# Kernel tuning notes

Measured on AMD Instinct MI355X. Metric: run time of the kernel, lower is better.

Reference implementation:

```python
import jax, jax.numpy as jnp
import numpy as np

H = 16
D_MODEL = 1024
D_HID = 50  # hidden width of the 1->50->1 mask MLP


def setup_inputs() -> dict:
    key = jax.random.key(0)
    ks = jax.random.split(key, 16)
    B, S, D = 16, 768, D_MODEL
    n, nk = 512, 256  # code length n, redundancy n-k; S = n + nk
    inp = {
        "query": jax.random.normal(ks[0], (B, S, D), jnp.float32),
        "key": jax.random.normal(ks[1], (B, S, D), jnp.float32),
        "value": jax.random.normal(ks[2], (B, S, D), jnp.float32),
        "pc_matrix": jax.random.uniform(ks[3], (nk, n), jnp.float32),
        # four Linear(d_model, d_model) layers: q, k, v, out. Stored so that y = x @ W + b.
        "Wq": jax.random.normal(ks[4], (D, D), jnp.float32) * 0.02,
        "bq": jnp.zeros((D,), jnp.float32),
        "Wk": jax.random.normal(ks[5], (D, D), jnp.float32) * 0.02,
        "bk": jnp.zeros((D,), jnp.float32),
        "Wv": jax.random.normal(ks[6], (D, D), jnp.float32) * 0.02,
        "bv": jnp.zeros((D,), jnp.float32),
        "Wo": jax.random.normal(ks[7], (D, D), jnp.float32) * 0.02,
        "bo": jnp.zeros((D,), jnp.float32),
        # one_d_mapping: Linear(1,50) -> ReLU -> Linear(50,1)
        "mw1": jax.random.normal(ks[8], (1, D_HID), jnp.float32) * 0.5,
        "mb1": jax.random.normal(ks[9], (D_HID,), jnp.float32) * 0.1,
        "mw2": jax.random.normal(ks[10], (D_HID, 1), jnp.float32) * 0.5,
        "mb2": jnp.zeros((1,), jnp.float32),
    }
    return inp


def _mask_from_pc(pc, mw1, mb1, mw2, mb2):
    # pc: (nk, n). Build (S, S) block matrix, S = n + nk.
    nknk = pc @ pc.T            # (nk, nk)
    nn = pc.T @ pc              # (n, n)
    top = jnp.concatenate([nn, pc.T], axis=1)     # (n, S)
    bot = jnp.concatenate([pc, nknk], axis=1)     # (nk, S)
    M = jnp.concatenate([top, bot], axis=0)       # (S, S)
    # elementwise 1->50->1 MLP
    h = jax.nn.relu(M[..., None] * mw1[0] + mb1)  # (S, S, 50)
    out = h @ mw2 + mb2                           # (S, S, 1)
    return out[..., 0]                            # (S, S)


def reference(query, key, value, pc_matrix, Wq, bq, Wk, bk, Wv, bv, Wo, bo,
              mw1, mb1, mw2, mb2):
    B, S, D = query.shape
    dk = D // H
    q = (query @ Wq + bq).reshape(B, S, H, dk).transpose(0, 2, 1, 3)
    k = (key @ Wk + bk).reshape(B, S, H, dk).transpose(0, 2, 1, 3)
    v = (value @ Wv + bv).reshape(B, S, H, dk).transpose(0, 2, 1, 3)
    scores = jnp.einsum("bhqd,bhkd->bhqk", q, k) / jnp.sqrt(jnp.float32(dk))
    mask = _mask_from_pc(pc_matrix, mw1, mb1, mw2, mb2)  # (S, S)
    scores = scores * mask[None, None]  # multiplicative float mask
    p = jax.nn.softmax(scores, axis=-1)  # dropout is identity in eval mode
    x = jnp.einsum("bhqk,bhkd->bhqd", p, v)
    x = x.transpose(0, 2, 1, 3).reshape(B, S, D)
    return x @ Wo + bo
```

## Files before the change

### kernel.cpp

```cpp
#include <hip/hip_runtime.h>
#include <stdint.h>

typedef _Float16 f16;
typedef _Float16 f16x8 __attribute__((ext_vector_type(8)));
typedef float f32x4 __attribute__((ext_vector_type(4)));

union U4 { uint4 u; f16 h[8]; };
union U2 { uint2 u; f16 h[4]; };

#define GLOAD16(g, l)                                                         \
  __builtin_amdgcn_global_load_lds(                                           \
      (const __attribute__((address_space(1))) void*)(g),                     \
      (__attribute__((address_space(3))) void*)(l), 16, 0, 0)

__global__ __launch_bounds__(256) void k_wt(const float* __restrict__ W0,
                                            const float* __restrict__ W1,
                                            const float* __restrict__ W2,
                                            const float* __restrict__ W3,
                                            f16* __restrict__ T0, f16* __restrict__ T1,
                                            f16* __restrict__ T2, f16* __restrict__ T3) {
    __shared__ f16 tile[64 * 65];
    int z = blockIdx.z;
    const float* W = z == 0 ? W0 : z == 1 ? W1 : z == 2 ? W2 : W3;
    f16* Wt = z == 0 ? T0 : z == 1 ? T1 : z == 2 ? T2 : T3;
    int t = threadIdx.x;
    int k0 = blockIdx.x * 64, n0 = blockIdx.y * 64;
    #pragma unroll
    for (int i = 0; i < 4; i++) {
        int cid = t + i * 256;
        int row = cid >> 4, c4 = cid & 15;
        float4 v = *(const float4*)(W + (size_t)(k0 + row) * 1024 + n0 + c4 * 4);
        tile[(c4 * 4 + 0) * 65 + row] = (f16)v.x;
        tile[(c4 * 4 + 1) * 65 + row] = (f16)v.y;
        tile[(c4 * 4 + 2) * 65 + row] = (f16)v.z;
        tile[(c4 * 4 + 3) * 65 + row] = (f16)v.w;
    }
    __syncthreads();
    #pragma unroll
    for (int i = 0; i < 2; i++) {
        int cid = t + i * 256;
        int nr = cid >> 3, kc = cid & 7;
        U4 u;
        #pragma unroll
        for (int j = 0; j < 8; j++) u.h[j] = tile[nr * 65 + kc * 8 + j];
        *(uint4*)(Wt + (size_t)(n0 + nr) * 1024 + k0 + kc * 8) = u.u;
    }
}

__global__ __launch_bounds__(256) void k_cvt(const float* __restrict__ in,
                                             f16* __restrict__ out) {
    size_t id = (size_t)blockIdx.x * 256 + threadIdx.x;
    float4 a = *(const float4*)(in + id * 8);
    float4 b = *(const float4*)(in + id * 8 + 4);
    U4 u;
    u.h[0] = (f16)a.x; u.h[1] = (f16)a.y; u.h[2] = (f16)a.z; u.h[3] = (f16)a.w;
    u.h[4] = (f16)b.x; u.h[5] = (f16)b.y; u.h[6] = (f16)b.z; u.h[7] = (f16)b.w;
    *(uint4*)(out + id * 8) = u.u;
}

template <int TRANS>
__global__ __launch_bounds__(256) void k_gram(const float* __restrict__ pc,
                                              float* __restrict__ out) {
    constexpr int N = TRANS ? 256 : 512;
    constexpr int K = TRANS ? 512 : 256;
    __shared__ float As[16][68];
    __shared__ float Bs[16][68];
    int t = threadIdx.x;
    int i0 = blockIdx.x * 64, j0 = blockIdx.y * 64;
    int ty = t >> 4, tx = t & 15;
    float acc[4][4];
    #pragma unroll
    for (int r = 0; r < 4; r++)
        #pragma unroll
        for (int c = 0; c < 4; c++) acc[r][c] = 0.f;

    for (int kt = 0; kt < K; kt += 16) {
        if (TRANS == 0) {
            int k = t >> 4, c4 = t & 15;
            float4 va = *(const float4*)(pc + (size_t)(kt + k) * 512 + i0 + c4 * 4);
            float4 vb = *(const float4*)(pc + (size_t)(kt + k) * 512 + j0 + c4 * 4);
            *(float4*)&As[k][c4 * 4] = va;
            *(float4*)&Bs[k][c4 * 4] = vb;
        } else {
            int r = t >> 2, kc = t & 3;
            float4 va = *(const float4*)(pc + (size_t)(i0 + r) * 512 + kt + kc * 4);
            As[kc * 4 + 0][r] = va.x; As[kc * 4 + 1][r] = va.y;
            As[kc * 4 + 2][r] = va.z; As[kc * 4 + 3][r] = va.w;
            float4 vb = *(const float4*)(pc + (size_t)(j0 + r) * 512 + kt + kc * 4);
            Bs[kc * 4 + 0][r] = vb.x; Bs[kc * 4 + 1][r] = vb.y;
            Bs[kc * 4 + 2][r] = vb.z; Bs[kc * 4 + 3][r] = vb.w;
        }
        __syncthreads();
        #pragma unroll
        for (int u = 0; u < 16; u++) {
            float4 av = *(const float4*)&As[u][ty * 4];
            float4 bv = *(const float4*)&Bs[u][tx * 4];
            float aa[4] = {av.x, av.y, av.z, av.w};
            float bb[4] = {bv.x, bv.y, bv.z, bv.w};
            #pragma unroll
            for (int r = 0; r < 4; r++)
                #pragma unroll
                for (int c = 0; c < 4; c++) acc[r][c] += aa[r] * bb[c];
        }
        __syncthreads();
    }
    #pragma unroll
    for (int r = 0; r < 4; r++)
        #pragma unroll
        for (int c = 0; c < 4; c++)
            out[(size_t)(i0 + ty * 4 + r) * N + j0 + tx * 4 + c] = acc[r][c];
}

__global__ __launch_bounds__(256) void k_mask(const float* __restrict__ pc,
                                              const float* __restrict__ nn,
                                              const float* __restrict__ nknk,
                                              const float* __restrict__ mw1,
                                              const float* __restrict__ mb1,
                                              const float* __restrict__ mw2,
                                              const float* __restrict__ mb2,
                                              float* __restrict__ maskp) {
    __shared__ float w1[50], b1[50], w2[50];
    int t = threadIdx.x;
    if (t < 50) { w1[t] = mw1[t]; b1[t] = mb1[t]; w2[t] = mw2[t]; }
    __syncthreads();
    int id = blockIdx.x * 256 + t;
    int i = id / 768, j = id - i * 768;
    float M;
    if (i < 512) M = (j < 512) ? nn[(size_t)i * 512 + j] : pc[(size_t)(j - 512) * 512 + i];
    else         M = (j < 512) ? pc[(size_t)(i - 512) * 512 + j]
                               : nknk[(size_t)(i - 512) * 256 + (j - 512)];
    float acc = mb2[0];
    #pragma unroll 10
    for (int u = 0; u < 50; u++) acc += fmaxf(M * w1[u] + b1[u], 0.f) * w2[u];
    maskp[id] = acc * 0.18033688011112042f;
}

__global__ __launch_bounds__(256) void k_vt(const f16* __restrict__ Vh,
                                            f16* __restrict__ VT) {
    __shared__ f16 tile[64][72];
    int t = threadIdx.x;
    int s0 = blockIdx.x * 64;
    int bh = blockIdx.y, b = bh >> 4, h = bh & 15;
    #pragma unroll
    for (int p = 0; p < 2; p++) {
        int cid = t + p * 256;
        int s = cid >> 3, dc = cid & 7;
        *(uint4*)&tile[s][dc * 8] =
            *(const uint4*)(Vh + ((size_t)b * 768 + s0 + s) * 1024 + h * 64 + dc * 8);
    }
    __syncthreads();
    #pragma unroll
    for (int p = 0; p < 2; p++) {
        int cid = t + p * 256;
        int d = cid >> 3, sc = cid & 7;
        U4 u;
        #pragma unroll
        for (int j = 0; j < 8; j++) u.h[j] = tile[sc * 8 + j][d];
        *(uint4*)(VT + ((size_t)bh * 64 + d) * 768 + s0 + sc * 8) = u.u;
    }
}

template <int MODE>
__global__ __launch_bounds__(256) void k_gemm(const f16* __restrict__ A,
                                              const f16* __restrict__ Bt,
                                              const float* __restrict__ bias,
                                              void* out0v, void* out1v) {
    __shared__ f16 As[128 * 32];
    __shared__ f16 Bs[128 * 32];
    int t = threadIdx.x;
    int w = t >> 6, lane = t & 63, l15 = lane & 15, quad = lane >> 4;
    int wm = w >> 1, wn = w & 1;
    int id = blockIdx.x;
    int rest = id >> 3;
    int row0 = ((id & 7) * 12 + rest % 12) * 128;
    int n0 = (rest / 12) * 128;

    int m0 = w * 16 + (lane >> 2);
    int m1 = m0 + 64;
    int ks0 = (lane & 3) ^ ((m0 >> 1) & 3);
    int ks1 = (lane & 3) ^ ((m1 >> 1) & 3);
    const f16* gA0 = A + (size_t)(row0 + m0) * 1024 + ks0 * 8;
    const f16* gA1 = A + (size_t)(row0 + m1) * 1024 + ks1 * 8;
    const f16* gB0 = Bt + (size_t)(n0 + m0) * 1024 + ks0 * 8;
    const f16* gB1 = Bt + (size_t)(n0 + m1) * 1024 + ks1 * 8;
    f16* lA = As + w * 512;
    f16* lB = Bs + w * 512;
    int sw = (l15 >> 1) & 3;

    f32x4 acc[4][4];
    #pragma unroll
    for (int mi = 0; mi < 4; mi++)
        #pragma unroll
        for (int ni = 0; ni < 4; ni++) acc[mi][ni] = (f32x4){0.f, 0.f, 0.f, 0.f};

    for (int kt = 0; kt < 32; kt++) {
        int k0 = kt * 32;
        GLOAD16(gA0 + k0, lA);
        GLOAD16(gA1 + k0, lA + 2048);
        GLOAD16(gB0 + k0, lB);
        GLOAD16(gB1 + k0, lB + 2048);
        __syncthreads();
        f16x8 af[4], bf_[4];
        #pragma unroll
        for (int mi = 0; mi < 4; mi++)
            af[mi] = *(const f16x8*)((const char*)As +
                     (size_t)(wm * 64 + mi * 16 + l15) * 64 + ((quad ^ sw) << 4));
        #pragma unroll
        for (int ni = 0; ni < 4; ni++)
            bf_[ni] = *(const f16x8*)((const char*)Bs +
                      (size_t)(wn * 64 + ni * 16 + l15) * 64 + ((quad ^ sw) << 4));
        #pragma unroll
        for (int mi = 0; mi < 4; mi++)
            #pragma unroll
            for (int ni = 0; ni < 4; ni++)
                acc[mi][ni] = __builtin_amdgcn_mfma_f32_16x16x32_f16(af[mi], bf_[ni],
                                                                     acc[mi][ni], 0, 0, 0);
        __syncthreads();
    }
    #pragma unroll
    for (int mi = 0; mi < 4; mi++) {
        #pragma unroll
        for (int ni = 0; ni < 4; ni++) {
            int col = n0 + wn * 64 + ni * 16 + l15;
            float bv = bias[col];
            #pragma unroll
            for (int r = 0; r < 4; r++) {
                int row = row0 + wm * 64 + mi * 16 + quad * 4 + r;
                float v = acc[mi][ni][r] + bv;
                size_t idx = (size_t)row * 1024 + col;
                if (MODE == 0) {
                    ((f16*)out0v)[idx] = (f16)v;
                } else if (MODE == 1) {
                    f16 hi = (f16)v;
                    ((f16*)out0v)[idx] = hi;
                    ((f16*)out1v)[idx] = (f16)(v - (float)hi);
                } else {
                    ((float*)out0v)[idx] = v;
                }
            }
        }
    }
}

__global__ __launch_bounds__(256) void k_attn(const f16* __restrict__ Qhi,
                                              const f16* __restrict__ Qlo,
                                              const f16* __restrict__ Khi,
                                              const f16* __restrict__ Klo,
                                              const f16* __restrict__ VT,
                                              const float* __restrict__ maskp,
                                              f16* __restrict__ Xout) {
    __shared__ f16 Ksh[2][64 * 64];
    __shared__ f16 Ksl[2][64 * 64];
    __shared__ f16 Vs[2][64 * 64];
    __shared__ f16 Ps[4][16 * 64];
    int t = threadIdx.x;
    int w = t >> 6, lane = t & 63, l15 = lane & 15, quad = lane >> 4;
    int id = blockIdx.x;
    int bh = (id & 7) + ((id >> 3) / 12) * 8;
    int q0 = ((id >> 3) % 12) * 64;
    int b = bh >> 4, h = bh & 15;
    const size_t base = ((size_t)b * 768) * 1024 + h * 64;

    int srow = lane >> 3;
    int sslot = lane & 7;

    f16x8 qh[2], ql[2];
    int qrow = q0 + w * 16 + l15;
    #pragma unroll
    for (int c = 0; c < 2; c++) {
        qh[c] = *(const f16x8*)(Qhi + base + (size_t)qrow * 1024 + c * 32 + quad * 8);
        ql[c] = *(const f16x8*)(Qlo + base + (size_t)qrow * 1024 + c * 32 + quad * 8);
    }
    float mrow = -1e30f, lrow = 0.f;
    f32x4 o[4];
    #pragma unroll
    for (int ni = 0; ni < 4; ni++) o[ni] = (f32x4){0.f, 0.f, 0.f, 0.f};

    auto STAGE = [&](int bsel, int k0) {
        #pragma unroll
        for (int p = 0; p < 2; p++) {
            int row = w * 16 + p * 8 + srow;
            int ss = sslot ^ (row & 7);
            GLOAD16(Khi + base + (size_t)(k0 + row) * 1024 + ss * 8,
                    &Ksh[bsel][w * 1024 + p * 512]);
            GLOAD16(Klo + base + (size_t)(k0 + row) * 1024 + ss * 8,
                    &Ksl[bsel][w * 1024 + p * 512]);
            GLOAD16(VT + ((size_t)bh * 64 + row) * 768 + k0 + ss * 8,
                    &Vs[bsel][w * 1024 + p * 512]);
        }
    };

    STAGE(0, 0);
    __syncthreads();
    int buf = 0;
    int kx = l15 & 7;
    const float* mbase = maskp + (size_t)quad * 4 * 768 + q0 + w * 16 + l15;

    for (int kt = 0; kt < 12; kt++) {
        int k0 = kt * 64;
        float mvs[4][4];
        #pragma unroll
        for (int kn = 0; kn < 4; kn++)
            #pragma unroll
            for (int r = 0; r < 4; r++)
                mvs[kn][r] = mbase[(size_t)(k0 + kn * 16 + r) * 768];
        if (kt < 11) STAGE(buf ^ 1, k0 + 64);

        float sv[4][4];
        #pragma unroll
        for (int kn = 0; kn < 4; kn++) {
            f32x4 s = (f32x4){0.f, 0.f, 0.f, 0.f};
            int key = kn * 16 + l15;
            #pragma unroll
            for (int c = 0; c < 2; c++) {
                int slot = ((c << 2) + quad) ^ kx;
                f16x8 kh = *(const f16x8*)((const char*)&Ksh[buf][0] +
                                           (size_t)key * 128 + (slot << 4));
                f16x8 kl = *(const f16x8*)((const char*)&Ksl[buf][0] +
                                           (size_t)key * 128 + (slot << 4));
                s = __builtin_amdgcn_mfma_f32_16x16x32_f16(kh, qh[c], s, 0, 0, 0);
                s = __builtin_amdgcn_mfma_f32_16x16x32_f16(kh, ql[c], s, 0, 0, 0);
                s = __builtin_amdgcn_mfma_f32_16x16x32_f16(kl, qh[c], s, 0, 0, 0);
            }
            #pragma unroll
            for (int r = 0; r < 4; r++) sv[kn][r] = s[r] * mvs[kn][r];
        }

        float tk0 = fmaxf(fmaxf(sv[0][0], sv[0][1]), fmaxf(sv[0][2], sv[0][3]));
        float tk1 = fmaxf(fmaxf(sv[1][0], sv[1][1]), fmaxf(sv[1][2], sv[1][3]));
        float tk2 = fmaxf(fmaxf(sv[2][0], sv[2][1]), fmaxf(sv[2][2], sv[2][3]));
        float tk3 = fmaxf(fmaxf(sv[3][0], sv[3][1]), fmaxf(sv[3][2], sv[3][3]));
        float tm = fmaxf(fmaxf(tk0, tk1), fmaxf(tk2, tk3));
        tm = fmaxf(tm, __shfl_xor(tm, 16));
        tm = fmaxf(tm, __shfl_xor(tm, 32));
        if (__any(tm > mrow + 11.0f)) {
            float mn = fmaxf(mrow, tm);
            float alpha = exp2f(mrow - mn);
            mrow = mn;
            lrow *= alpha;
            #pragma unroll
            for (int ni = 0; ni < 4; ni++)
                #pragma unroll
                for (int r = 0; r < 4; r++) o[ni][r] *= alpha;
        }
        float rs = 0.f;
        #pragma unroll
        for (int kn = 0; kn < 4; kn++) {
            U2 pk;
            #pragma unroll
            for (int r = 0; r < 4; r++) {
                float pv = exp2f(sv[kn][r] - mrow);
                rs += pv;
                pk.h[r] = (f16)pv;
            }
            int slot = (kn * 2 + (quad >> 1)) ^ kx;
            *(uint2*)((char*)&Ps[w][0] + l15 * 128 + (slot << 4) + ((quad & 1) << 3)) = pk.u;
        }
        rs += __shfl_xor(rs, 16);
        rs += __shfl_xor(rs, 32);
        lrow += rs;

        asm volatile("s_waitcnt lgkmcnt(0)" ::: "memory");
        __builtin_amdgcn_sched_barrier(0);
        #pragma unroll
        for (int c = 0; c < 2; c++) {
            int pslot = ((c << 2) + quad) ^ kx;
            f16x8 pa = *(const f16x8*)((const char*)&Ps[w][0] +
                                       (size_t)l15 * 128 + (pslot << 4));
            #pragma unroll
            for (int ni = 0; ni < 4; ni++) {
                int d = ni * 16 + l15;
                f16x8 vb = *(const f16x8*)((const char*)&Vs[buf][0] +
                                           (size_t)d * 128 + (pslot << 4));
                o[ni] = __builtin_amdgcn_mfma_f32_16x16x32_f16(vb, pa, o[ni], 0, 0, 0);
            }
        }
        __syncthreads();
        buf ^= 1;
    }
    float rl = 1.0f / lrow;
    int qg = q0 + w * 16 + l15;
    #pragma unroll
    for (int ni = 0; ni < 4; ni++) {
        U2 ok;
        #pragma unroll
        for (int r = 0; r < 4; r++) ok.h[r] = (f16)(o[ni][r] * rl);
        *(uint2*)(Xout + ((size_t)b * 768 + qg) * 1024 + h * 64 + ni * 16 + quad * 4) = ok.u;
    }
}

extern "C" void kernel_launch(void* const* d_in, const int* in_sizes, int n_in,
                              void* d_out, int out_size, void* d_ws, size_t ws_size,
                              hipStream_t stream) {
    (void)in_sizes; (void)n_in; (void)out_size; (void)ws_size;
    const float* query = (const float*)d_in[0];
    const float* key   = (const float*)d_in[1];
    const float* value = (const float*)d_in[2];
    const float* pc    = (const float*)d_in[3];
    const float* Wq    = (const float*)d_in[4];
    const float* bq    = (const float*)d_in[5];
    const float* Wk    = (const float*)d_in[6];
    const float* bk    = (const float*)d_in[7];
    const float* Wv    = (const float*)d_in[8];
    const float* bv    = (const float*)d_in[9];
    const float* Wo    = (const float*)d_in[10];
    const float* bo    = (const float*)d_in[11];
    const float* mw1   = (const float*)d_in[12];
    const float* mb1   = (const float*)d_in[13];
    const float* mw2   = (const float*)d_in[14];
    const float* mb2   = (const float*)d_in[15];

    char* p = (char*)d_ws;
    auto take = [&](size_t bytes) -> char* {
        char* r = p; p += (bytes + 255) & ~(size_t)255; return r;
    };
    const size_t NTOK = 12288, DM = 1024;
    float* maskb = (float*)take(768 * 768 * 4);
    float* nnb   = (float*)take(512 * 512 * 4);
    float* nknkb = (float*)take(256 * 256 * 4);
    f16* Wqt = (f16*)take(DM * DM * 2);
    f16* Wkt = (f16*)take(DM * DM * 2);
    f16* Wvt = (f16*)take(DM * DM * 2);
    f16* Wot = (f16*)take(DM * DM * 2);
    f16* buf1 = (f16*)take(NTOK * DM * 2);
    f16* Qhi = (f16*)take(NTOK * DM * 2);
    f16* Qlo = (f16*)take(NTOK * DM * 2);
    f16* Khi = (f16*)take(NTOK * DM * 2);
    f16* Klo = (f16*)take(NTOK * DM * 2);
    f16* Vhb = (f16*)take(NTOK * DM * 2);
    f16* VTb = (f16*)take(NTOK * DM * 2);

    k_wt<<<dim3(16, 16, 4), 256, 0, stream>>>(Wq, Wk, Wv, Wo, Wqt, Wkt, Wvt, Wot);
    k_gram<0><<<dim3(8, 8), 256, 0, stream>>>(pc, nnb);
    k_gram<1><<<dim3(4, 4), 256, 0, stream>>>(pc, nknkb);
    k_mask<<<2304, 256, 0, stream>>>(pc, nnb, nknkb, mw1, mb1, mw2, mb2, maskb);

    k_cvt<<<6144, 256, 0, stream>>>(query, buf1);
    k_gemm<1><<<768, 256, 0, stream>>>(buf1, Wqt, bq, Qhi, Qlo);
    k_cvt<<<6144, 256, 0, stream>>>(key, buf1);
    k_gemm<1><<<768, 256, 0, stream>>>(buf1, Wkt, bk, Khi, Klo);
    k_cvt<<<6144, 256, 0, stream>>>(value, buf1);
    k_gemm<0><<<768, 256, 0, stream>>>(buf1, Wvt, bv, Vhb, nullptr);

    k_vt<<<dim3(12, 256), 256, 0, stream>>>(Vhb, VTb);

    k_attn<<<3072, 256, 0, stream>>>(Qhi, Qlo, Khi, Klo, VTb, maskb, buf1);

    k_gemm<2><<<768, 256, 0, stream>>>(buf1, Wot, bo, d_out, nullptr);
}
```

Measured before the change: 606.6 us.

## Single-buffer V tile and load it within the iteration to cut LDS

The V tile now uses one LDS buffer instead of a double buffer, and each iteration loads it for the current step, overlapped with the QK MFMAs and softmax. Explicit vmcnt waits and raw s_barrier calls replace __syncthreads so the PV stage waits only for V while the next K load stays in flight. The smaller LDS footprint may allow more blocks per CU, but V latency is now exposed within the iteration and an extra barrier is added. The max reduction is also regrouped into three-way fmax chains.

After: 577.3 us. 4.8% less time.

```diff
diff --git a/kernel.cpp b/kernel.cpp
--- a/kernel.cpp
+++ b/kernel.cpp
@@ -251,7 +251,7 @@
                                               f16* __restrict__ Xout) {
     __shared__ f16 Ksh[2][64 * 64];
     __shared__ f16 Ksl[2][64 * 64];
-    __shared__ f16 Vs[2][64 * 64];
+    __shared__ f16 Vs[64 * 64];
     __shared__ f16 Ps[4][16 * 64];
     int t = threadIdx.x;
     int w = t >> 6, lane = t & 63, l15 = lane & 15, quad = lane >> 4;
@@ -276,7 +276,7 @@
     #pragma unroll
     for (int ni = 0; ni < 4; ni++) o[ni] = (f32x4){0.f, 0.f, 0.f, 0.f};
 
-    auto STAGE = [&](int bsel, int k0) {
+    auto STAGE_K = [&](int bsel, int k0) {
         #pragma unroll
         for (int p = 0; p < 2; p++) {
             int row = w * 16 + p * 8 + srow;
@@ -285,13 +285,21 @@
                     &Ksh[bsel][w * 1024 + p * 512]);
             GLOAD16(Klo + base + (size_t)(k0 + row) * 1024 + ss * 8,
                     &Ksl[bsel][w * 1024 + p * 512]);
+        }
+    };
+    auto STAGE_V = [&](int k0) {
+        #pragma unroll
+        for (int p = 0; p < 2; p++) {
+            int row = w * 16 + p * 8 + srow;
+            int ss = sslot ^ (row & 7);
             GLOAD16(VT + ((size_t)bh * 64 + row) * 768 + k0 + ss * 8,
-                    &Vs[bsel][w * 1024 + p * 512]);
+                    &Vs[w * 1024 + p * 512]);
         }
     };
 
-    STAGE(0, 0);
-    __syncthreads();
+    STAGE_K(0, 0);
+    asm volatile("s_waitcnt vmcnt(0)" ::: "memory");
+    __builtin_amdgcn_s_barrier();
     int buf = 0;
     int kx = l15 & 7;
     const float* mbase = maskp + (size_t)quad * 4 * 768 + q0 + w * 16 + l15;
@@ -304,7 +312,8 @@
             #pragma unroll
             for (int r = 0; r < 4; r++)
                 mvs[kn][r] = mbase[(size_t)(k0 + kn * 16 + r) * 768];
-        if (kt < 11) STAGE(buf ^ 1, k0 + 64);
+        STAGE_V(k0);
+        if (kt < 11) STAGE_K(buf ^ 1, k0 + 64);
 
         float sv[4][4];
         #pragma unroll
@@ -326,11 +335,12 @@
             for (int r = 0; r < 4; r++) sv[kn][r] = s[r] * mvs[kn][r];
         }
 
-        float tk0 = fmaxf(fmaxf(sv[0][0], sv[0][1]), fmaxf(sv[0][2], sv[0][3]));
-        float tk1 = fmaxf(fmaxf(sv[1][0], sv[1][1]), fmaxf(sv[1][2], sv[1][3]));
-        float tk2 = fmaxf(fmaxf(sv[2][0], sv[2][1]), fmaxf(sv[2][2], sv[2][3]));
-        float tk3 = fmaxf(fmaxf(sv[3][0], sv[3][1]), fmaxf(sv[3][2], sv[3][3]));
-        float tm = fmaxf(fmaxf(tk0, tk1), fmaxf(tk2, tk3));
+        float g0 = fmaxf(fmaxf(sv[0][0], sv[0][1]), sv[0][2]);
+        float g1 = fmaxf(fmaxf(sv[0][3], sv[1][0]), sv[1][1]);
+        float g2 = fmaxf(fmaxf(sv[1][2], sv[1][3]), sv[2][0]);
+        float g3 = fmaxf(fmaxf(sv[2][1], sv[2][2]), sv[2][3]);
+        float g4 = fmaxf(fmaxf(sv[3][0], sv[3][1]), sv[3][2]);
+        float tm = fmaxf(fmaxf(fmaxf(g0, g1), fmaxf(g2, g3)), fmaxf(g4, sv[3][3]));
         tm = fmaxf(tm, __shfl_xor(tm, 16));
         tm = fmaxf(tm, __shfl_xor(tm, 32));
         if (__any(tm > mrow + 11.0f)) {
@@ -361,6 +371,9 @@
         lrow += rs;
 
         asm volatile("s_waitcnt lgkmcnt(0)" ::: "memory");
+        if (kt < 11) asm volatile("s_waitcnt vmcnt(4)" ::: "memory");
+        else         asm volatile("s_waitcnt vmcnt(0)" ::: "memory");
+        __builtin_amdgcn_s_barrier();
         __builtin_amdgcn_sched_barrier(0);
         #pragma unroll
         for (int c = 0; c < 2; c++) {
@@ -370,12 +383,13 @@
             #pragma unroll
             for (int ni = 0; ni < 4; ni++) {
                 int d = ni * 16 + l15;
-                f16x8 vb = *(const f16x8*)((const char*)&Vs[buf][0] +
+                f16x8 vb = *(const f16x8*)((const char*)&Vs[0] +
                                            (size_t)d * 128 + (pslot << 4));
                 o[ni] = __builtin_amdgcn_mfma_f32_16x16x32_f16(vb, pa, o[ni], 0, 0, 0);
             }
         }
-        __syncthreads();
+        asm volatile("s_waitcnt vmcnt(0)" ::: "memory");
+        __builtin_amdgcn_s_barrier();
         buf ^= 1;
     }
     float rl = 1.0f / lrow;
```
